# Optimization experiments

Measured on AMD Instinct MI355X. Metric: run time of the kernel, lower is better.

The kernel has to match this reference:

```python
import jax, jax.numpy as jnp
import numpy as np

NEG = -1e30  # finite stand-in for -inf so logsumexp grads stay finite


def ctc_loss_mean(y_true, log_probs_tm, input_length, label_length, blank=0):
    """CTC loss (forward algorithm in log space), mean over batch.

    log_probs_tm: [T, B, C] time-major log-probabilities.
    y_true:       [B, L] dense int labels (blank=0 excluded from real labels).
    """
    T, B, C = log_probs_tm.shape
    L = y_true.shape[1]
    S = 2 * L + 1  # extended label length: blank, l1, blank, l2, ...
    ll = jnp.clip(label_length, 1, L)
    il = jnp.clip(input_length, 1, T)

    # Extended label sequence: blanks at even positions, labels at odd.
    ext = jnp.full((B, S), blank, dtype=jnp.int32).at[:, 1::2].set(y_true.astype(jnp.int32))
    ext_m2 = jnp.concatenate([jnp.full((B, 2), -1, jnp.int32), ext[:, :-2]], axis=1)
    # Skip transition (s-2 -> s) allowed only for label positions with no repeat.
    allow_skip = ((jnp.arange(S) % 2 == 1)[None, :]) & (ext != ext_m2)

    lp0 = jnp.take_along_axis(log_probs_tm[0], ext, axis=1)  # [B, S]
    alpha0 = jnp.full((B, S), NEG, log_probs_tm.dtype)
    alpha0 = alpha0.at[:, 0].set(lp0[:, 0]).at[:, 1].set(lp0[:, 1])

    def step(alpha, xs):
        lp_t, t = xs
        lpe = jnp.take_along_axis(lp_t, ext, axis=1)  # [B, S]
        a1 = jnp.concatenate([jnp.full((B, 1), NEG, alpha.dtype), alpha[:, :-1]], axis=1)
        a2 = jnp.concatenate([jnp.full((B, 2), NEG, alpha.dtype), alpha[:, :-2]], axis=1)
        a2 = jnp.where(allow_skip, a2, NEG)
        new = jax.nn.logsumexp(jnp.stack([alpha, a1, a2]), axis=0) + lpe
        # Freeze alpha once past each example's input_length.
        return jnp.where((t < il)[:, None], new, alpha), None

    alpha, _ = jax.lax.scan(step, alpha0, (log_probs_tm[1:], jnp.arange(1, T)))

    # Loss = -log(alpha[2*ll-1] + alpha[2*ll]) at the final (frozen) time step.
    idx = jnp.stack([2 * ll - 1, 2 * ll], axis=1)  # [B, 2]
    end_vals = jnp.take_along_axis(alpha, idx, axis=1)
    loss = -jax.nn.logsumexp(end_vals, axis=1)
    return jnp.mean(loss)


def setup_inputs() -> dict:
    key = jax.random.key(0)
    kx, kl, ki, kj = jax.random.split(key, 4)
    B, T, C, L = 64, 1024, 128, 256
    # y_pred are probabilities (module applies log), so softmax random logits.
    y_pred = jax.nn.softmax(jax.random.normal(kx, (B, T, C), jnp.float32), axis=-1)
    y_true = jax.random.randint(kl, (B, L), 1, C, jnp.int32)  # blank=0 excluded
    input_length = jax.random.randint(ki, (B,), T // 2, T + 1, jnp.int32)
    label_length = jax.random.randint(kj, (B,), L // 2, L + 1, jnp.int32)
    return {"y_true": y_true, "y_pred": y_pred,
            "input_length": input_length, "label_length": label_length}


def reference(y_true, y_pred, input_length, label_length):
    # Mirror CTCLayer.call: log + transpose to time-major, reshape lengths.
    log_tm = jnp.log(jnp.transpose(y_pred, (1, 0, 2)))  # [T, B, C]
    loss = ctc_loss_mean(y_true, log_tm,
                         input_length.reshape(-1), label_length.reshape(-1),
                         blank=0)
    return log_tm, loss
```

## Files before the change

kernel.cpp:

```cpp
#include <hip/hip_runtime.h>
#include <math.h>

constexpr int B = 64;
constexpr int T = 1024;
constexpr int C = 128;
constexpr int L = 256;
constexpr int S = 2 * L + 1;
constexpr int TRB = 2048;
constexpr int N4 = T * B * C / 4;

template <int N> struct IC { static constexpr int value = N; };

__global__ __launch_bounds__(64, 1) void ctc_fused(
    const float* __restrict__ yp,
    const int*   __restrict__ yt,
    const int*   __restrict__ il_,
    const int*   __restrict__ ll_,
    float* __restrict__ out_log,
    float* __restrict__ out_loss)
{
    if (blockIdx.x >= B) {
        int gid = (blockIdx.x - B) * 64 + threadIdx.x;
        const float4* in4 = (const float4*)yp;
        float4* o4 = (float4*)out_log;
        for (int i = gid; i < N4; i += TRB * 64) {
            int c4 = i & 31;
            int tb = i >> 5;
            int bb = tb & 63;
            int tt = tb >> 6;
            float4 v = in4[(bb * T + tt) * 32 + c4];
            float4 r;
            r.x = __logf(v.x); r.y = __logf(v.y);
            r.z = __logf(v.z); r.w = __logf(v.w);
            o4[i] = r;
        }
        return;
    }

    const int b    = blockIdx.x;
    const int lane = threadIdx.x;

    __shared__ float lsh[1536];
    __shared__ float afin[S];

    int il = il_[b]; il = min(max(il, 1), T);
    int ll = ll_[b]; ll = min(max(ll, 1), L);
    const float* yb = yp + (size_t)b * T * C;

    int4 y4  = *(const int4*)(yt + b * L + 4 * lane);
    int  po  = lane ? 4 * lane - 4 : 0;
    int4 py4 = *(const int4*)(yt + b * L + po);
    int  ppw = yt[b * L + (lane >= 2 ? 4 * lane - 5 : 0)];

    int lab[8]   = {py4.x, py4.y, py4.z, py4.w, y4.x, y4.y, y4.z, y4.w};
    int labm1[8] = {ppw,   py4.x, py4.y, py4.z, py4.w, y4.x, y4.y, y4.z};
    float skf[8];
    #pragma unroll
    for (int k = 0; k < 8; ++k)
        skf[k] = ((4 * lane + k >= 5) && (lab[k] != labm1[k])) ? 1.f : 0.f;

    auto ldpair = [&](int m) -> float4 {
        int r = 2 * m + 1 + (lane >> 5);
        r = r > T - 1 ? T - 1 : r;
        return ((const float4*)(yb + r * C))[lane & 31];
    };

    float p00 = yb[0];
    float p0l = yb[y4.x];
    float4 w01 = ldpair(0), w23 = ldpair(1);
    float4 w45 = ldpair(2), w67 = ldpair(3);
    float4 prr[8];
    #pragma unroll
    for (int m = 4; m <= 11; ++m) prr[m & 7] = ldpair(m);

    ((float4*)(lsh +   0))[lane] = w01;
    ((float4*)(lsh + 256))[lane] = w23;
    ((float4*)(lsh + 512))[lane] = w45;
    ((float4*)(lsh + 768))[lane] = w67;

    int b_cur = 0, b_nxt = 512, b_stg = 1024;
    int t0 = 0;

    float gvo[2][4][8], gvb[2][4];
    #pragma unroll
    for (int j = 0; j < 4; ++j) {
        const float* rp = lsh + j * 128;
        gvb[0][j] = rp[0];
        #pragma unroll
        for (int k = 1; k < 8; ++k) gvo[0][j][k] = rp[lab[k]];
    }

    float w[17];
    #pragma unroll
    for (int i = 0; i < 17; ++i) w[i] = 0.f;
    if (lane == 0) { w[8] = p00; w[9] = p0l; }

    auto halo = [&]() {
        #pragma unroll
        for (int k = 0; k < 8; ++k) {
            float h = __shfl_up(w[8 + k], 1);
            w[k] = lane ? h : 0.f;
        }
    };
    halo();

    float ls = 0.f;
    float m_meas = 1.0f;

    auto group = [&](auto Pc, auto S0c) {
        constexpr int P  = decltype(Pc)::value;
        constexpr int S0 = decltype(S0c)::value;
        #pragma unroll
        for (int j = 0; j < 4; ++j) {
            const float* rp = lsh + b_nxt + j * 128;
            gvb[P ^ 1][j] = rp[0];
            #pragma unroll
            for (int k = 1; k < 8; ++k) gvo[P ^ 1][j][k] = rp[lab[k]];
        }
        ((float4*)(lsh + b_stg      ))[lane] = prr[S0];
        ((float4*)(lsh + b_stg + 256))[lane] = prr[S0 + 1];
        prr[S0]     = ldpair((t0 >> 1) + 12);
        prr[S0 + 1] = ldpair((t0 >> 1) + 13);
        #pragma unroll
        for (int j = 0; j < 4; ++j) {
            #pragma unroll
            for (int i = 16; i >= 2 * (j + 1); --i) {
                float acc = w[i] + w[i - 1];
                float g;
                if (i & 1) {
                    acc = fmaf(skf[(i - 1) >> 1], w[i - 2], acc);
                    g = gvo[P][j][(i - 1) >> 1];
                } else {
                    g = gvb[P][j];
                }
                w[i] = acc * g;
            }
        }
        int tb = b_cur; b_cur = b_nxt; b_nxt = b_stg; b_stg = tb;
        t0 += 4;
    };

    auto rescale = [&](float mm) {
        int eb = (__float_as_int(mm) >> 23) & 0xff;
        int sh = 350 - eb;
        sh = sh > 254 ? 254 : (sh < 1 ? 1 : sh);
        float inv = __int_as_float(sh << 23);
        #pragma unroll
        for (int i = 8; i < 17; ++i) w[i] *= inv;
        ls -= (float)(sh - 127);
    };
    auto maxw = [&]() {
        return fmaxf(fmaxf(fmaxf(w[8], w[9]), fmaxf(w[10], w[11])),
                     fmaxf(fmaxf(w[12], w[13]),
                           fmaxf(fmaxf(w[14], w[15]), w[16])));
    };

    const int full_end = ((il - 1) >> 2) << 2;

    while (t0 + 16 <= full_end) {
        float mm = m_meas;
        mm = fmaxf(mm, __shfl_xor(mm, 1));
        mm = fmaxf(mm, __shfl_xor(mm, 2));
        mm = fmaxf(mm, __shfl_xor(mm, 4));
        group(IC<0>{}, IC<4>{});
        halo();
        mm = fmaxf(mm, __shfl_xor(mm, 8));
        mm = fmaxf(mm, __shfl_xor(mm, 16));
        mm = fmaxf(mm, __shfl_xor(mm, 32));
        group(IC<1>{}, IC<6>{});
        rescale(mm);
        m_meas = maxw();
        halo();

        float m2 = m_meas;
        m2 = fmaxf(m2, __shfl_xor(m2, 1));
        m2 = fmaxf(m2, __shfl_xor(m2, 2));
        m2 = fmaxf(m2, __shfl_xor(m2, 4));
        group(IC<0>{}, IC<0>{});
        halo();
        m2 = fmaxf(m2, __shfl_xor(m2, 8));
        m2 = fmaxf(m2, __shfl_xor(m2, 16));
        m2 = fmaxf(m2, __shfl_xor(m2, 32));
        group(IC<1>{}, IC<2>{});
        rescale(m2);
        m_meas = maxw();
        halo();
    }
    if (t0 + 4 <= full_end) { group(IC<0>{}, IC<4>{}); halo(); }
    if (t0 + 4 <= full_end) { group(IC<1>{}, IC<6>{}); halo(); }
    if (t0 + 4 <= full_end) { group(IC<0>{}, IC<0>{}); }

    for (int r = full_end + 1; r < il; ++r) {
        const float* rp = lsh + b_cur + ((r - 1) & 3) * 128;
        float hh = __shfl_up(w[15], 1); if (lane == 0) hh = 0.f;
        float gb = rp[0];
        float n8  = (w[8] + hh) * gb;
        float n9  = fmaf(skf[4], hh,    w[9]  + w[8])  * rp[y4.x];
        float n10 = (w[10] + w[9])  * gb;
        float n11 = fmaf(skf[5], w[9],  w[11] + w[10]) * rp[y4.y];
        float n12 = (w[12] + w[11]) * gb;
        float n13 = fmaf(skf[6], w[11], w[13] + w[12]) * rp[y4.z];
        float n14 = (w[14] + w[13]) * gb;
        float n15 = fmaf(skf[7], w[13], w[15] + w[14]) * rp[y4.w];
        float n16 = (w[16] + w[15]) * gb;
        w[8] = n8;  w[9] = n9;  w[10] = n10; w[11] = n11; w[12] = n12;
        w[13] = n13; w[14] = n14; w[15] = n15; w[16] = n16;
    }

    #pragma unroll
    for (int k = 0; k < 8; ++k) afin[8 * lane + k] = w[8 + k];
    if (lane == 63) afin[512] = w[16];
    __syncthreads();
    if (lane == 0) {
        float e1 = afin[2 * ll - 1];
        float e2 = afin[2 * ll];
        float sum = fmaxf(e1 + e2, 1e-37f);
        float loss = -(__log2f(sum) + ls) * 0.6931471805599453f;
        atomicAdd(out_loss, loss * (1.0f / (float)B));
    }
}

extern "C" void kernel_launch(void* const* d_in, const int* in_sizes, int n_in,
                              void* d_out, int out_size, void* d_ws, size_t ws_size,
                              hipStream_t stream) {
    const int*   y_true = (const int*)d_in[0];
    const float* y_pred = (const float*)d_in[1];
    const int*   in_len = (const int*)d_in[2];
    const int*   lb_len = (const int*)d_in[3];

    float* out_log  = (float*)d_out;
    float* out_loss = (float*)d_out + (size_t)T * B * C;

    hipMemsetAsync(out_loss, 0, sizeof(float), stream);
    ctc_fused<<<B + TRB, 64, 0, stream>>>(y_pred, y_true, in_len, lb_len,
                                          out_log, out_loss);
}
```

Baseline: 198.1 us.

## Gather label probabilities directly from global into registers with 4-deep prefetch

Replaces the shared-memory staging of full probability rows with direct per-lane global gathers of each lane's four label probabilities, prefetched three groups ahead in a rotating register buffer. Blank probabilities for all timesteps are preloaded once into shared memory, and the neighbour-lane label values come via shuffles. The aim is to drop the shared-memory row copies and LDS gathers from the serial recurrence loop. In exchange it issues scattered scalar global loads, uses more registers, and adds extra rescales in the tail groups.

```diff
diff --git a/kernel.cpp b/kernel.cpp
--- a/kernel.cpp
+++ b/kernel.cpp
@@ -40,7 +40,7 @@
     const int b    = blockIdx.x;
     const int lane = threadIdx.x;
 
-    __shared__ float lsh[1536];
+    __shared__ float blanks[T];
     __shared__ float afin[S];
 
     int il = il_[b]; il = min(max(il, 1), T);
@@ -59,36 +59,27 @@
     for (int k = 0; k < 8; ++k)
         skf[k] = ((4 * lane + k >= 5) && (lab[k] != labm1[k])) ? 1.f : 0.f;
 
-    auto ldpair = [&](int m) -> float4 {
-        int r = 2 * m + 1 + (lane >> 5);
-        r = r > T - 1 ? T - 1 : r;
-        return ((const float4*)(yb + r * C))[lane & 31];
-    };
+    const int c0 = y4.x, c1 = y4.y, c2 = y4.z, c3 = y4.w;
+
+    #pragma unroll
+    for (int i = 0; i < T / 64; ++i)
+        blanks[i * 64 + lane] = yb[(size_t)(i * 64 + lane) * C];
 
     float p00 = yb[0];
-    float p0l = yb[y4.x];
-    float4 w01 = ldpair(0), w23 = ldpair(1);
-    float4 w45 = ldpair(2), w67 = ldpair(3);
-    float4 prr[8];
-    #pragma unroll
-    for (int m = 4; m <= 11; ++m) prr[m & 7] = ldpair(m);
-
-    ((float4*)(lsh +   0))[lane] = w01;
-    ((float4*)(lsh + 256))[lane] = w23;
-    ((float4*)(lsh + 512))[lane] = w45;
-    ((float4*)(lsh + 768))[lane] = w67;
-
-    int b_cur = 0, b_nxt = 512, b_stg = 1024;
-    int t0 = 0;
-
-    float gvo[2][4][8], gvb[2][4];
-    #pragma unroll
-    for (int j = 0; j < 4; ++j) {
-        const float* rp = lsh + j * 128;
-        gvb[0][j] = rp[0];
-        #pragma unroll
-        for (int k = 1; k < 8; ++k) gvo[0][j][k] = rp[lab[k]];
-    }
+    float p0l = yb[c0];
+
+    float gvL[4][4][4];
+    auto ldgrp = [&](auto Sc, int g) {
+        constexpr int SL = decltype(Sc)::value;
+        #pragma unroll
+        for (int j = 0; j < 4; ++j) {
+            int r = 4 * g + 1 + j; r = r > T - 1 ? T - 1 : r;
+            const float* rp = yb + (size_t)r * C;
+            gvL[SL][j][0] = rp[c0]; gvL[SL][j][1] = rp[c1];
+            gvL[SL][j][2] = rp[c2]; gvL[SL][j][3] = rp[c3];
+        }
+    };
+    ldgrp(IC<0>{}, 0); ldgrp(IC<1>{}, 1); ldgrp(IC<2>{}, 2);
 
     float w[17];
     #pragma unroll
@@ -106,21 +97,30 @@
 
     float ls = 0.f;
     float m_meas = 1.0f;
-
-    auto group = [&](auto Pc, auto S0c) {
+    int t0 = 0;
+
+    auto group = [&](auto Pc) {
         constexpr int P  = decltype(Pc)::value;
-        constexpr int S0 = decltype(S0c)::value;
+        constexpr int PN = (P + 3) & 3;
+        {
+            #pragma unroll
+            for (int j = 0; j < 4; ++j) {
+                int r = t0 + 13 + j; r = r > T - 1 ? T - 1 : r;
+                const float* rp = yb + (size_t)r * C;
+                gvL[PN][j][0] = rp[c0]; gvL[PN][j][1] = rp[c1];
+                gvL[PN][j][2] = rp[c2]; gvL[PN][j][3] = rp[c3];
+            }
+        }
+        float gvp1[4], gvp2[4], gvp3[4];
         #pragma unroll
         for (int j = 0; j < 4; ++j) {
-            const float* rp = lsh + b_nxt + j * 128;
-            gvb[P ^ 1][j] = rp[0];
-            #pragma unroll
-            for (int k = 1; k < 8; ++k) gvo[P ^ 1][j][k] = rp[lab[k]];
-        }
-        ((float4*)(lsh + b_stg      ))[lane] = prr[S0];
-        ((float4*)(lsh + b_stg + 256))[lane] = prr[S0 + 1];
-        prr[S0]     = ldpair((t0 >> 1) + 12);
-        prr[S0 + 1] = ldpair((t0 >> 1) + 13);
+            gvp1[j] = __shfl_up(gvL[P][j][1], 1);
+            gvp2[j] = __shfl_up(gvL[P][j][2], 1);
+            gvp3[j] = __shfl_up(gvL[P][j][3], 1);
+        }
+        float gb[4];
+        #pragma unroll
+        for (int j = 0; j < 4; ++j) gb[j] = blanks[t0 + 1 + j];
         #pragma unroll
         for (int j = 0; j < 4; ++j) {
             #pragma unroll
@@ -128,15 +128,17 @@
                 float acc = w[i] + w[i - 1];
                 float g;
                 if (i & 1) {
-                    acc = fmaf(skf[(i - 1) >> 1], w[i - 2], acc);
-                    g = gvo[P][j][(i - 1) >> 1];
+                    constexpr_int:;
+                    const int k = (i - 1) >> 1;
+                    acc = fmaf(skf[k], w[i - 2], acc);
+                    g = (k >= 4) ? gvL[P][j][k - 4]
+                                 : (k == 1 ? gvp1[j] : (k == 2 ? gvp2[j] : gvp3[j]));
                 } else {
-                    g = gvb[P][j];
+                    g = gb[j];
                 }
                 w[i] = acc * g;
             }
         }
-        int tb = b_cur; b_cur = b_nxt; b_nxt = b_stg; b_stg = tb;
         t0 += 4;
     };
 
@@ -162,12 +164,12 @@
         mm = fmaxf(mm, __shfl_xor(mm, 1));
         mm = fmaxf(mm, __shfl_xor(mm, 2));
         mm = fmaxf(mm, __shfl_xor(mm, 4));
-        group(IC<0>{}, IC<4>{});
+        group(IC<0>{});
         halo();
         mm = fmaxf(mm, __shfl_xor(mm, 8));
         mm = fmaxf(mm, __shfl_xor(mm, 16));
         mm = fmaxf(mm, __shfl_xor(mm, 32));
-        group(IC<1>{}, IC<6>{});
+        group(IC<1>{});
         rescale(mm);
         m_meas = maxw();
         halo();
@@ -176,35 +178,65 @@
         m2 = fmaxf(m2, __shfl_xor(m2, 1));
         m2 = fmaxf(m2, __shfl_xor(m2, 2));
         m2 = fmaxf(m2, __shfl_xor(m2, 4));
-        group(IC<0>{}, IC<0>{});
+        group(IC<2>{});
         halo();
         m2 = fmaxf(m2, __shfl_xor(m2, 8));
         m2 = fmaxf(m2, __shfl_xor(m2, 16));
         m2 = fmaxf(m2, __shfl_xor(m2, 32));
-        group(IC<1>{}, IC<2>{});
+        group(IC<3>{});
         rescale(m2);
         m_meas = maxw();
         halo();
     }
-    if (t0 + 4 <= full_end) { group(IC<0>{}, IC<4>{}); halo(); }
-    if (t0 + 4 <= full_end) { group(IC<1>{}, IC<6>{}); halo(); }
-    if (t0 + 4 <= full_end) { group(IC<0>{}, IC<0>{}); }
-
-    for (int r = full_end + 1; r < il; ++r) {
-        const float* rp = lsh + b_cur + ((r - 1) & 3) * 128;
-        float hh = __shfl_up(w[15], 1); if (lane == 0) hh = 0.f;
-        float gb = rp[0];
-        float n8  = (w[8] + hh) * gb;
-        float n9  = fmaf(skf[4], hh,    w[9]  + w[8])  * rp[y4.x];
-        float n10 = (w[10] + w[9])  * gb;
-        float n11 = fmaf(skf[5], w[9],  w[11] + w[10]) * rp[y4.y];
-        float n12 = (w[12] + w[11]) * gb;
-        float n13 = fmaf(skf[6], w[11], w[13] + w[12]) * rp[y4.z];
-        float n14 = (w[14] + w[13]) * gb;
-        float n15 = fmaf(skf[7], w[13], w[15] + w[14]) * rp[y4.w];
-        float n16 = (w[16] + w[15]) * gb;
-        w[8] = n8;  w[9] = n9;  w[10] = n10; w[11] = n11; w[12] = n12;
-        w[13] = n13; w[14] = n14; w[15] = n15; w[16] = n16;
+
+    auto fresh_rescale = [&]() {
+        float mm = maxw();
+        #pragma unroll
+        for (int off = 1; off < 64; off <<= 1) mm = fmaxf(mm, __shfl_xor(mm, off));
+        rescale(mm);
+    };
+    if (t0 + 4 <= full_end) { group(IC<0>{}); fresh_rescale(); halo(); }
+    if (t0 + 4 <= full_end) { group(IC<1>{}); fresh_rescale(); halo(); }
+    if (t0 + 4 <= full_end) { group(IC<2>{}); }
+
+    const int ph = (full_end >> 2) & 3;
+    float tg[3][4];
+    switch (ph) {
+    case 0:
+        #pragma unroll
+        for (int j = 0; j < 3; ++j) { tg[j][0]=gvL[0][j][0]; tg[j][1]=gvL[0][j][1]; tg[j][2]=gvL[0][j][2]; tg[j][3]=gvL[0][j][3]; }
+        break;
+    case 1:
+        #pragma unroll
+        for (int j = 0; j < 3; ++j) { tg[j][0]=gvL[1][j][0]; tg[j][1]=gvL[1][j][1]; tg[j][2]=gvL[1][j][2]; tg[j][3]=gvL[1][j][3]; }
+        break;
+    case 2:
+        #pragma unroll
+        for (int j = 0; j < 3; ++j) { tg[j][0]=gvL[2][j][0]; tg[j][1]=gvL[2][j][1]; tg[j][2]=gvL[2][j][2]; tg[j][3]=gvL[2][j][3]; }
+        break;
+    default:
+        #pragma unroll
+        for (int j = 0; j < 3; ++j) { tg[j][0]=gvL[3][j][0]; tg[j][1]=gvL[3][j][1]; tg[j][2]=gvL[3][j][2]; tg[j][3]=gvL[3][j][3]; }
+        break;
+    }
+    #pragma unroll
+    for (int j = 0; j < 3; ++j) {
+        int r = full_end + 1 + j;
+        if (r < il) {
+            float hh = __shfl_up(w[15], 1); if (lane == 0) hh = 0.f;
+            float gb = blanks[r];
+            float n8  = (w[8] + hh) * gb;
+            float n9  = fmaf(skf[4], hh,    w[9]  + w[8])  * tg[j][0];
+            float n10 = (w[10] + w[9])  * gb;
+            float n11 = fmaf(skf[5], w[9],  w[11] + w[10]) * tg[j][1];
+            float n12 = (w[12] + w[11]) * gb;
+            float n13 = fmaf(skf[6], w[11], w[13] + w[12]) * tg[j][2];
+            float n14 = (w[14] + w[13]) * gb;
+            float n15 = fmaf(skf[7], w[13], w[15] + w[14]) * tg[j][3];
+            float n16 = (w[16] + w[15]) * gb;
+            w[8] = n8;  w[9] = n9;  w[10] = n10; w[11] = n11; w[12] = n12;
+            w[13] = n13; w[14] = n14; w[15] = n15; w[16] = n16;
+        }
     }
 
     #pragma unroll
```

Result: no change. 201.3 us (+1.6%).
